# Kernel optimization log

Measured on AMD Instinct MI355X. Metric: run time of the kernel, lower is better.

The kernel has to match this reference:

```python
import jax, jax.numpy as jnp
import numpy as np

N_NODES = 50000
D = 128
L = 3  # layers
R = 4  # relations
E = 200000  # edges per relation
LN_EPS = 1e-5
NEG_SLOPE = 0.2


def setup_inputs() -> dict:
    key = jax.random.key(0)
    ks = jax.random.split(key, 12)
    s = 1.0 / np.sqrt(D)  # xavier-ish scale
    return {
        "h": jax.random.normal(ks[0], (N_NODES, D), jnp.float32),
        "edge_src": jax.random.randint(ks[1], (R, E), 0, N_NODES, jnp.int32),
        "edge_dst": jax.random.randint(ks[2], (R, E), 0, N_NODES, jnp.int32),
        "W_src": jax.random.normal(ks[3], (L, R, D, D), jnp.float32) * s,
        "W_dst": jax.random.normal(ks[4], (L, R, D, D), jnp.float32) * s,
        "attn_l": jax.random.normal(ks[5], (L, R, D), jnp.float32) * s,
        "attn_r": jax.random.normal(ks[6], (L, R, D), jnp.float32) * s,
        "gat_bias": jax.random.normal(ks[7], (L, R, D), jnp.float32) * 0.02,
        "ntype_bias": jax.random.normal(ks[8], (L, D), jnp.float32) * 0.02,
        "ln_gamma": jnp.ones((L, D), jnp.float32),
        "ln_beta": jnp.zeros((L, D), jnp.float32),
    }


def _gat_rel(x, Wsrc, Wdst, al, ar, b, src, dst):
    # single-head DGL GATConv with bipartite (src, dst) feats (same node set here)
    n = x.shape[0]
    hs = x @ Wsrc  # [N, D] projected source feats
    hd = x @ Wdst  # [N, D] projected dest feats
    el = (hs * al).sum(-1)  # [N]
    er = (hd * ar).sum(-1)  # [N]
    e = jax.nn.leaky_relu(el[src] + er[dst], NEG_SLOPE)  # [E]
    # edge softmax over incoming edges of each dst node
    m = jax.lax.stop_gradient(jax.ops.segment_max(e, dst, num_segments=n))
    a = jnp.exp(e - m[dst])
    denom = jax.ops.segment_sum(a, dst, num_segments=n)
    w = a / denom[dst]  # [E] attention weights
    out = jax.ops.segment_sum(hs[src] * w[:, None], dst, num_segments=n)  # [N, D]
    return out + b


def _layer_norm(x, g, b):
    mu = x.mean(-1, keepdims=True)
    var = ((x - mu) ** 2).mean(-1, keepdims=True)
    return (x - mu) * jax.lax.rsqrt(var + LN_EPS) * g + b


def reference(h, edge_src, edge_dst, W_src, W_dst, attn_l, attn_r,
              gat_bias, ntype_bias, ln_gamma, ln_beta):
    x = h
    n_layers = W_src.shape[0]
    gat_vmapped = jax.vmap(_gat_rel, in_axes=(None, 0, 0, 0, 0, 0, 0, 0))
    for l in range(n_layers):
        rel_out = gat_vmapped(x, W_src[l], W_dst[l], attn_l[l], attn_r[l],
                              gat_bias[l], edge_src, edge_dst)  # [R, N, D]
        hsum = rel_out.sum(0) + ntype_bias[l]  # HeteroGraphConv 'sum' + ntype bias
        if l < n_layers - 1:
            hsum = jax.nn.relu(hsum)  # activation on all but final layer
        # mean over heads (num_heads=1) is identity; then per-layer LayerNorm
        x = _layer_norm(hsum, ln_gamma[l], ln_beta[l])
    return x
```

## Files before the change

### kernel.cpp

```cpp
#include <hip/hip_runtime.h>

#define NN 50000
#define DIM 128
#define NREL 4
#define NEDGE 200000
#define NLAYER 3
#define SNB 196
#define GR 128
#define NTILE (NN / 16)

typedef short s16x8 __attribute__((ext_vector_type(8)));
typedef float f32x4 __attribute__((ext_vector_type(4)));

__device__ __forceinline__ unsigned short f2bf(float f) {
    union { float f; unsigned u; } c; c.f = f;
    unsigned u = c.u + 0x7fffu + ((c.u >> 16) & 1u);
    return (unsigned short)(u >> 16);
}
__device__ __forceinline__ float lo_bf(unsigned u) {
    union { float f; unsigned u; } c; c.u = u << 16; return c.f;
}
__device__ __forceinline__ float hi_bf(unsigned u) {
    union { float f; unsigned u; } c; c.u = u & 0xffff0000u; return c.f;
}

__global__ __launch_bounds__(256) void k_constf(float* __restrict__ out, int n, float v) {
    int i = blockIdx.x * 256 + threadIdx.x;
    if (i < n) out[i] = v;
}

__global__ __launch_bounds__(256) void k_count(const int* __restrict__ dst, int* __restrict__ counts) {
    int r = blockIdx.y;
    int i = blockIdx.x * 256 + threadIdx.x;
    if (i < NEDGE) {
        int d = dst[r * NEDGE + i];
        if ((unsigned)d < NN) atomicAdd(&counts[r * NN + d], 1);
    }
}

__global__ __launch_bounds__(256) void k_s1(const int* __restrict__ counts, int* __restrict__ bsum) {
    int r = blockIdx.y, b = blockIdx.x;
    int i = b * 256 + threadIdx.x;
    int v = (i < NN) ? counts[r * NN + i] : 0;
    #pragma unroll
    for (int m = 1; m < 64; m <<= 1) v += __shfl_xor(v, m);
    __shared__ int ws[4];
    int wid = threadIdx.x >> 6, lane = threadIdx.x & 63;
    if (lane == 0) ws[wid] = v;
    __syncthreads();
    if (threadIdx.x == 0) bsum[r * SNB + b] = ws[0] + ws[1] + ws[2] + ws[3];
}

__global__ __launch_bounds__(256) void k_s2(const int* __restrict__ bsum, int* __restrict__ boff) {
    int r = threadIdx.x >> 6;
    int lane = threadIdx.x & 63;
    int carry = 0;
    for (int c0 = 0; c0 < SNB; c0 += 64) {
        int b = c0 + lane;
        int v = (b < SNB) ? bsum[r * SNB + b] : 0;
        int inc = v;
        #pragma unroll
        for (int d = 1; d < 64; d <<= 1) {
            int t = __shfl_up(inc, d);
            if (lane >= d) inc += t;
        }
        if (b < SNB) boff[r * SNB + b] = carry + inc - v;
        carry += __shfl(inc, 63);
    }
}

__global__ __launch_bounds__(256) void k_s3(const int* __restrict__ counts, const int* __restrict__ boff,
                                            int* __restrict__ row_ptr, int* __restrict__ nxt) {
    int r = blockIdx.y, b = blockIdx.x;
    int i = b * 256 + threadIdx.x;
    int v = (i < NN) ? counts[r * NN + i] : 0;
    int lane = threadIdx.x & 63, wid = threadIdx.x >> 6;
    int inc = v;
    #pragma unroll
    for (int d = 1; d < 64; d <<= 1) {
        int t = __shfl_up(inc, d);
        if (lane >= d) inc += t;
    }
    __shared__ int ws[4];
    if (lane == 63) ws[wid] = inc;
    __syncthreads();
    int woff = 0;
    #pragma unroll
    for (int w = 0; w < 4; ++w) woff += (w < wid) ? ws[w] : 0;
    if (i < NN) {
        int ex = boff[r * SNB + b] + woff + inc - v;
        row_ptr[r * (NN + 1) + i] = ex;
        nxt[r * NN + i] = ex;
    }
    if (b == 0 && threadIdx.x == 0) row_ptr[r * (NN + 1) + NN] = NEDGE;
}

__global__ __launch_bounds__(256) void k_fill(const int* __restrict__ src, const int* __restrict__ dst,
                                              int* __restrict__ nxt, int* __restrict__ csr) {
    int r = blockIdx.y;
    int i = blockIdx.x * 256 + threadIdx.x;
    if (i < NEDGE) {
        int d = dst[r * NEDGE + i];
        if ((unsigned)d >= NN) return;
        int pos = atomicAdd(&nxt[r * NN + d], 1);
        if ((unsigned)pos < NEDGE) csr[r * NEDGE + pos] = src[r * NEDGE + i];
    }
}

__global__ __launch_bounds__(256) void k_prep(const float* __restrict__ Wsrc,
                                              const float* __restrict__ Wdst,
                                              const float* __restrict__ al,
                                              const float* __restrict__ ar,
                                              const float* __restrict__ ntb,
                                              const float* __restrict__ gb,
                                              const float* __restrict__ x,
                                              unsigned short* __restrict__ wf,
                                              float* __restrict__ wl,
                                              float* __restrict__ wr,
                                              float* __restrict__ biasc,
                                              unsigned short* __restrict__ xb) {
    int b = blockIdx.x;
    const int PL = NLAYER * 512;
    if (b < PL) {
        int l = b / 512;
        int t = b % 512;
        if (t < 256) {
            int idx = t * 256 + threadIdx.x;
            int jj = idx & 7, lane = (idx >> 3) & 63, s = (idx >> 9) & 3, tt = (idx >> 11) & 7, r = idx >> 14;
            int k = s * 32 + ((lane >> 4) << 3) + jj;
            int n = tt * 16 + (lane & 15);
            wf[l * 65536 + idx] = f2bf(Wsrc[((size_t)(l * NREL + r) * DIM + k) * DIM + n]);
        } else if (t < 384) {
            int gw = (t - 256) * 4 + (threadIdx.x >> 6);
            int lane = threadIdx.x & 63;
            int r = gw >> 7, k = gw & 127;
            const float* wrow = Wsrc + (((size_t)(l * NREL + r) * DIM + k) * DIM);
            const float* arow = al + (l * NREL + r) * DIM;
            float s = wrow[lane * 2] * arow[lane * 2] + wrow[lane * 2 + 1] * arow[lane * 2 + 1];
            #pragma unroll
            for (int m = 1; m < 64; m <<= 1) s += __shfl_xor(s, m);
            if (lane == 0) wl[l * 512 + gw] = s;
        } else {
            int gw = (t - 384) * 4 + (threadIdx.x >> 6);
            int lane = threadIdx.x & 63;
            int r = gw >> 7, k = gw & 127;
            const float* wrow = Wdst + (((size_t)(l * NREL + r) * DIM + k) * DIM);
            const float* arow = ar + (l * NREL + r) * DIM;
            float s = wrow[lane * 2] * arow[lane * 2] + wrow[lane * 2 + 1] * arow[lane * 2 + 1];
            #pragma unroll
            for (int m = 1; m < 64; m <<= 1) s += __shfl_xor(s, m);
            if (lane == 0) wr[l * 512 + gw] = s;
        }
    } else if (b < PL + 2) {
        int t = (b - PL) * 256 + threadIdx.x;
        if (t < NLAYER * DIM) {
            int l = t >> 7, k = t & 127;
            float s = ntb[t];
            #pragma unroll
            for (int r = 0; r < NREL; ++r) s += gb[(l * NREL + r) * DIM + k];
            biasc[t] = s;
        }
    } else {
        int i = ((b - PL - 2) * 256 + threadIdx.x) * 4;
        f32x4 v = *(const f32x4*)(x + i);
        unsigned short o[4];
        #pragma unroll
        for (int j = 0; j < 4; ++j) o[j] = f2bf(v[j]);
        *(ushort2*)(xb + i) = make_ushort2(o[0], o[1]);
        *(ushort2*)(xb + i + 2) = make_ushort2(o[2], o[3]);
    }
}

__global__ __launch_bounds__(256) void k_er0(const float* __restrict__ x,
                                             const float* __restrict__ wl,
                                             const float* __restrict__ wr,
                                             float* __restrict__ el,
                                             float* __restrict__ er) {
    int oct = threadIdx.x >> 3, ol = threadIdx.x & 7;
    int n = blockIdx.x * 32 + oct;
    if (n >= NN) return;
    int f0 = ol * 16;
    const float* xp = x + (size_t)n * DIM + f0;
    f32x4 xv[4];
    #pragma unroll
    for (int k = 0; k < 4; ++k) xv[k] = *(const f32x4*)(xp + 4 * k);
    #pragma unroll
    for (int r = 0; r < NREL; ++r) {
        float sl = 0.f, sr = 0.f;
        #pragma unroll
        for (int k = 0; k < 4; ++k) {
            f32x4 lv = *(const f32x4*)(wl + r * DIM + f0 + 4 * k);
            f32x4 rv = *(const f32x4*)(wr + r * DIM + f0 + 4 * k);
            sl += xv[k][0] * lv[0] + xv[k][1] * lv[1] + xv[k][2] * lv[2] + xv[k][3] * lv[3];
            sr += xv[k][0] * rv[0] + xv[k][1] * rv[1] + xv[k][2] * rv[2] + xv[k][3] * rv[3];
        }
        sl += __shfl_xor(sl, 1); sl += __shfl_xor(sl, 2); sl += __shfl_xor(sl, 4);
        sr += __shfl_xor(sr, 1); sr += __shfl_xor(sr, 2); sr += __shfl_xor(sr, 4);
        if (ol == 0) { el[r * NN + n] = sl; er[r * NN + n] = sr; }
    }
}

__global__ __launch_bounds__(256) void k_gather(const unsigned short* __restrict__ xb,
                                                const float* __restrict__ el,
                                                const float* __restrict__ er,
                                                const int* __restrict__ row_ptr,
                                                const int* __restrict__ csr,
                                                unsigned short* __restrict__ aggf) {
    int gid = blockIdx.x * 256 + threadIdx.x;
    int ol = gid & 3;
    int p  = gid >> 2;
    int n  = p >> 2;
    int r  = p & 3;
    if (n >= NN) return;
    int f0 = ol * 32;

    int start = row_ptr[r * (NN + 1) + n];
    int end   = row_ptr[r * (NN + 1) + n + 1];
    if (start < 0) start = 0;
    if (end > NEDGE) end = NEDGE;
    int deg = end - start;

    float ern = er[r * NN + n];
    const int* cp = csr + r * NEDGE;
    const float* elp = el + r * NN;

    f32x4 av[8] = {{0,0,0,0},{0,0,0,0},{0,0,0,0},{0,0,0,0},
                   {0,0,0,0},{0,0,0,0},{0,0,0,0},{0,0,0,0}};
    float denom = 0.f;
    if (deg > 0) {
        int s0 = cp[start]; if ((unsigned)s0 >= NN) s0 = 0;
        float e0 = elp[s0];
        const uint4* hp = (const uint4*)(xb + (size_t)s0 * DIM + f0);
        uint4 xa = hp[0], xbv = hp[1], xc = hp[2], xd = hp[3];
        for (int e = 0; e < deg; ++e) {
            int i1 = start + e + 1; i1 = (i1 < end) ? i1 : start;
            int s1 = cp[i1]; if ((unsigned)s1 >= NN) s1 = 0;
            float e1 = elp[s1];
            const uint4* hp1 = (const uint4*)(xb + (size_t)s1 * DIM + f0);
            uint4 ya = hp1[0], yb = hp1[1], yc = hp1[2], yd = hp1[3];

            float ev = e0 + ern;
            ev = ev >= 0.f ? ev : 0.2f * ev;
            ev = fminf(fmaxf(ev, -60.f), 60.f);
            float pw = __expf(ev);
            denom += pw;
            av[0][0] += pw * lo_bf(xa.x); av[0][1] += pw * hi_bf(xa.x);
            av[0][2] += pw * lo_bf(xa.y); av[0][3] += pw * hi_bf(xa.y);
            av[1][0] += pw * lo_bf(xa.z); av[1][1] += pw * hi_bf(xa.z);
            av[1][2] += pw * lo_bf(xa.w); av[1][3] += pw * hi_bf(xa.w);
            av[2][0] += pw * lo_bf(xbv.x); av[2][1] += pw * hi_bf(xbv.x);
            av[2][2] += pw * lo_bf(xbv.y); av[2][3] += pw * hi_bf(xbv.y);
            av[3][0] += pw * lo_bf(xbv.z); av[3][1] += pw * hi_bf(xbv.z);
            av[3][2] += pw * lo_bf(xbv.w); av[3][3] += pw * hi_bf(xbv.w);
            av[4][0] += pw * lo_bf(xc.x); av[4][1] += pw * hi_bf(xc.x);
            av[4][2] += pw * lo_bf(xc.y); av[4][3] += pw * hi_bf(xc.y);
            av[5][0] += pw * lo_bf(xc.z); av[5][1] += pw * hi_bf(xc.z);
            av[5][2] += pw * lo_bf(xc.w); av[5][3] += pw * hi_bf(xc.w);
            av[6][0] += pw * lo_bf(xd.x); av[6][1] += pw * hi_bf(xd.x);
            av[6][2] += pw * lo_bf(xd.y); av[6][3] += pw * hi_bf(xd.y);
            av[7][0] += pw * lo_bf(xd.z); av[7][1] += pw * hi_bf(xd.z);
            av[7][2] += pw * lo_bf(xd.w); av[7][3] += pw * hi_bf(xd.w);
            e0 = e1; xa = ya; xbv = yb; xc = yc; xd = yd;
        }
    }
    float inv = (deg > 0) ? (1.0f / denom) : 0.f;
    s16x8* ap = (s16x8*)aggf + ((size_t)(n >> 4) * 16 + (r * 4 + ol)) * 64 + (n & 15);
    #pragma unroll
    for (int q = 0; q < 4; ++q) {
        s16x8 o;
        #pragma unroll
        for (int j = 0; j < 4; ++j) {
            o[j]     = (short)f2bf(av[2 * q][j] * inv);
            o[j + 4] = (short)f2bf(av[2 * q + 1][j] * inv);
        }
        ap[q * 16] = o;
    }
}

__global__ __launch_bounds__(256) void k_gemm(const unsigned short* __restrict__ aggf,
                                              const unsigned short* __restrict__ wf,
                                              const float* __restrict__ biasc,
                                              const float* __restrict__ lng,
                                              const float* __restrict__ lnb,
                                              const float* __restrict__ wl,
                                              const float* __restrict__ wr,
                                              float* __restrict__ dout,
                                              unsigned short* __restrict__ xb2,
                                              float* __restrict__ el2,
                                              float* __restrict__ er2,
                                              int l, int last) {
    __shared__ float Cl[GR * DIM];
    int tid = threadIdx.x;
    int wv = tid >> 6, lane = tid & 63;
    int quad = lane >> 4, n16 = lane & 15;
    int tile0 = blockIdx.x * (GR / 16);

    f32x4 acc0[8], acc1[8];
    #pragma unroll
    for (int rt = 0; rt < 8; ++rt) {
        acc0[rt] = (f32x4){0.f, 0.f, 0.f, 0.f};
        acc1[rt] = (f32x4){0.f, 0.f, 0.f, 0.f};
    }
    {
        const s16x8* wfp = (const s16x8*)wf + (size_t)l * NREL * 2048;
        const s16x8* af = (const s16x8*)aggf;
        int t0c = wv * 2, t1c = wv * 2 + 1;
        for (int sp = 0; sp < 16; ++sp) {
            const s16x8* wb = wfp + (size_t)(sp >> 2) * 2048;
            int sl = sp & 3;
            s16x8 b0 = wb[(t0c * 4 + sl) * 64 + lane];
            s16x8 b1 = wb[(t1c * 4 + sl) * 64 + lane];
            #pragma unroll
            for (int rt = 0; rt < 8; ++rt) {
                int tile = tile0 + rt;
                if (tile >= NTILE) tile = 0;
                s16x8 a = af[((size_t)tile * 16 + sp) * 64 + lane];
                acc0[rt] = __builtin_amdgcn_mfma_f32_16x16x32_bf16(a, b0, acc0[rt], 0, 0, 0);
                acc1[rt] = __builtin_amdgcn_mfma_f32_16x16x32_bf16(a, b1, acc1[rt], 0, 0, 0);
            }
        }
    }
    {
        int t0c = wv * 2, t1c = wv * 2 + 1;
        #pragma unroll
        for (int rt = 0; rt < 8; ++rt) {
            #pragma unroll
            for (int reg = 0; reg < 4; ++reg) {
                int row = rt * 16 + quad * 4 + reg;
                Cl[row * DIM + t0c * 16 + n16] = acc0[rt][reg];
                Cl[row * DIM + t1c * 16 + n16] = acc1[rt][reg];
            }
        }
    }
    __syncthreads();

    for (int it = 0; it < GR / 8; ++it) {
        int nd2 = it * 8 + (tid >> 5);
        int sub = tid & 31;
        int f   = sub * 4;
        int n2  = blockIdx.x * GR + nd2;
        if (n2 >= NN) continue;

        float t[4];
        #pragma unroll
        for (int j = 0; j < 4; ++j) t[j] = Cl[nd2 * DIM + f + j] + biasc[l * DIM + f + j];
        if (!last) {
            #pragma unroll
            for (int j = 0; j < 4; ++j) t[j] = fmaxf(t[j], 0.f);
        }
        float s1 = 0.f;
        #pragma unroll
        for (int j = 0; j < 4; ++j) s1 += t[j];
        s1 += __shfl_xor(s1, 1); s1 += __shfl_xor(s1, 2);
        s1 += __shfl_xor(s1, 4); s1 += __shfl_xor(s1, 8);
        s1 += __shfl_xor(s1, 16);
        float mean = s1 * (1.0f / 128.0f);
        float s2 = 0.f;
        #pragma unroll
        for (int j = 0; j < 4; ++j) { t[j] -= mean; s2 += t[j] * t[j]; }
        s2 += __shfl_xor(s2, 1); s2 += __shfl_xor(s2, 2);
        s2 += __shfl_xor(s2, 4); s2 += __shfl_xor(s2, 8);
        s2 += __shfl_xor(s2, 16);
        float rs = rsqrtf(s2 * (1.0f / 128.0f) + 1e-5f);

        float y[4];
        #pragma unroll
        for (int j = 0; j < 4; ++j)
            y[j] = t[j] * rs * lng[l * DIM + f + j] + lnb[l * DIM + f + j];

        if (last) {
            float* op = dout + (size_t)n2 * DIM + f;
            f32x4 v0;
            v0[0] = y[0]; v0[1] = y[1]; v0[2] = y[2]; v0[3] = y[3];
            *(f32x4*)op = v0;
        } else {
            unsigned pk0 = (unsigned)f2bf(y[0]) | ((unsigned)f2bf(y[1]) << 16);
            unsigned pk1 = (unsigned)f2bf(y[2]) | ((unsigned)f2bf(y[3]) << 16);
            uint2 v; v.x = pk0; v.y = pk1;
            *(uint2*)(xb2 + (size_t)n2 * DIM + f) = v;

            const float* wlp = wl + (l + 1) * 512;
            const float* wrp = wr + (l + 1) * 512;
            #pragma unroll
            for (int rp = 0; rp < NREL; ++rp) {
                float sl_ = 0.f, sr_ = 0.f;
                #pragma unroll
                for (int j = 0; j < 4; ++j) {
                    sl_ += y[j] * wlp[rp * DIM + f + j];
                    sr_ += y[j] * wrp[rp * DIM + f + j];
                }
                sl_ += __shfl_xor(sl_, 1); sl_ += __shfl_xor(sl_, 2);
                sl_ += __shfl_xor(sl_, 4); sl_ += __shfl_xor(sl_, 8);
                sl_ += __shfl_xor(sl_, 16);
                sr_ += __shfl_xor(sr_, 1); sr_ += __shfl_xor(sr_, 2);
                sr_ += __shfl_xor(sr_, 4); sr_ += __shfl_xor(sr_, 8);
                sr_ += __shfl_xor(sr_, 16);
                if (sub == 0) {
                    el2[rp * NN + n2] = sl_;
                    er2[rp * NN + n2] = sr_;
                }
            }
        }
    }
}

extern "C" void kernel_launch(void* const* d_in, const int* in_sizes, int n_in,
                              void* d_out, int out_size, void* d_ws, size_t ws_size,
                              hipStream_t stream) {
    const float* h        = (const float*)d_in[0];
    const int*   edge_src = (const int*)d_in[1];
    const int*   edge_dst = (const int*)d_in[2];
    const float* W_src    = (const float*)d_in[3];
    const float* W_dst    = (const float*)d_in[4];
    const float* attn_l   = (const float*)d_in[5];
    const float* attn_r   = (const float*)d_in[6];
    const float* gat_bias = (const float*)d_in[7];
    const float* ntype_b  = (const float*)d_in[8];
    const float* ln_g     = (const float*)d_in[9];
    const float* ln_b     = (const float*)d_in[10];

    if (n_in < 11) return;
    if (in_sizes[0] != NN * DIM) return;
    if (in_sizes[1] != NREL * NEDGE || in_sizes[2] != NREL * NEDGE) return;
    if (in_sizes[3] != NLAYER * NREL * DIM * DIM || in_sizes[4] != NLAYER * NREL * DIM * DIM) return;
    if (in_sizes[5] != NLAYER * NREL * DIM || in_sizes[6] != NLAYER * NREL * DIM) return;
    if (in_sizes[7] != NLAYER * NREL * DIM || in_sizes[8] != NLAYER * DIM) return;
    if (out_size != NN * DIM) return;

    auto align256 = [](size_t x) { return (x + 255) & ~(size_t)255; };
    size_t szElEr = align256((size_t)NREL * NN * 4);
    size_t szXbf  = align256((size_t)NN * DIM * 2);
    size_t szWlr  = align256((size_t)NLAYER * 512 * 4);
    size_t szBc   = align256((size_t)NLAYER * DIM * 4);
    size_t szWf   = align256((size_t)NLAYER * NREL * DIM * DIM * 2);
    size_t szRp   = align256((size_t)NREL * (NN + 1) * 4);
    size_t szNxt  = align256((size_t)NREL * NN * 4);
    size_t szCsr  = align256((size_t)NREL * NEDGE * 4);
    size_t szScn  = align256((size_t)NREL * SNB * 4) * 2;
    size_t szAgg  = align256((size_t)NN * 512 * 2);
    size_t need = 4 * szElEr + 2 * szXbf + 2 * szWlr + szBc + szWf + szRp + szNxt + szCsr + szScn + szAgg;

    if (ws_size < need) {
        k_constf<<<(NN * DIM + 255) / 256, 256, 0, stream>>>((float*)d_out, NN * DIM, 100.0f);
        return;
    }

    char* base = (char*)d_ws;
    size_t off = 0;
    auto alloc = [&](size_t bytes) -> char* { char* p = base + off; off += align256(bytes); return p; };

    float* el   = (float*)alloc((size_t)NREL * NN * 4);
    float* er   = (float*)alloc((size_t)NREL * NN * 4);
    float* el2  = (float*)alloc((size_t)NREL * NN * 4);
    float* er2  = (float*)alloc((size_t)NREL * NN * 4);
    unsigned short* xbf  = (unsigned short*)alloc((size_t)NN * DIM * 2);
    unsigned short* xbf2 = (unsigned short*)alloc((size_t)NN * DIM * 2);
    float* wl    = (float*)alloc((size_t)NLAYER * 512 * 4);
    float* wr    = (float*)alloc((size_t)NLAYER * 512 * 4);
    float* biasc = (float*)alloc((size_t)NLAYER * DIM * 4);
    unsigned short* wfrag = (unsigned short*)alloc((size_t)NLAYER * NREL * DIM * DIM * 2);
    int* rowp = (int*)alloc((size_t)NREL * (NN + 1) * 4);
    int* nxt  = (int*)alloc((size_t)NREL * NN * 4);
    int* csr  = (int*)alloc((size_t)NREL * NEDGE * 4);
    int* bsum = (int*)alloc((size_t)NREL * SNB * 4);
    int* boff = (int*)alloc((size_t)NREL * SNB * 4);
    unsigned short* aggf = (unsigned short*)alloc((size_t)NN * 512 * 2);

    (void)hipMemsetAsync(nxt, 0, (size_t)NREL * NN * 4, stream);
    k_count<<<dim3((NEDGE + 255) / 256, NREL), 256, 0, stream>>>(edge_dst, nxt);
    k_s1<<<dim3(SNB, NREL), 256, 0, stream>>>(nxt, bsum);
    k_s2<<<1, 256, 0, stream>>>(bsum, boff);
    k_s3<<<dim3(SNB, NREL), 256, 0, stream>>>(nxt, boff, rowp, nxt);
    k_fill<<<dim3((NEDGE + 255) / 256, NREL), 256, 0, stream>>>(edge_src, edge_dst, nxt, csr);
    k_prep<<<NLAYER * 512 + 2 + NN * DIM / 1024, 256, 0, stream>>>(
        W_src, W_dst, attn_l, attn_r, ntype_b, gat_bias, h, wfrag, wl, wr, biasc, xbf);
    k_er0<<<(NN + 31) / 32, 256, 0, stream>>>(h, wl, wr, el, er);

    float* dout = (float*)d_out;
    const int GATHER_BLK = (NN * NREL * 4 + 255) / 256;
    const int GEMM_BLK   = (NN + GR - 1) / GR;

    k_gather<<<GATHER_BLK, 256, 0, stream>>>(xbf, el, er, rowp, csr, aggf);
    k_gemm<<<GEMM_BLK, 256, 0, stream>>>(aggf, wfrag, biasc, ln_g, ln_b, wl, wr,
                                         dout, xbf2, el2, er2, 0, 0);
    k_gather<<<GATHER_BLK, 256, 0, stream>>>(xbf2, el2, er2, rowp, csr, aggf);
    k_gemm<<<GEMM_BLK, 256, 0, stream>>>(aggf, wfrag, biasc, ln_g, ln_b, wl, wr,
                                         dout, xbf, el, er, 1, 0);
    k_gather<<<GATHER_BLK, 256, 0, stream>>>(xbf, el, er, rowp, csr, aggf);
    k_gemm<<<GEMM_BLK, 256, 0, stream>>>(aggf, wfrag, biasc, ln_g, ln_b, wl, wr,
                                         dout, xbf2, el2, er2, 2, 1);
}
```

Measured before the change: 434.2 us.

## Give each wave a full 16-row tile and fuse LayerNorm on accumulators

The GEMM kernel now assigns one 16-node tile per wave that covers all 128 output columns, instead of each block computing 128 rows with waves splitting columns. Bias, ReLU, LayerNorm and the attention dot products are done directly from MFMA accumulator registers using 16-lane shuffles, so the 64KB shared-memory staging buffer and the block barrier go away. This raises occupancy and removes the LDS round-trip. In exchange, every wave reloads the whole weight matrix from cache instead of sharing it across 8 row tiles, and the output stores become strided 2- and 4-byte writes rather than vectorised ones.

```diff
diff --git a/kernel.cpp b/kernel.cpp
--- a/kernel.cpp
+++ b/kernel.cpp
@@ -6,7 +6,6 @@
 #define NEDGE 200000
 #define NLAYER 3
 #define SNB 196
-#define GR 128
 #define NTILE (NN / 16)
 
 typedef short s16x8 __attribute__((ext_vector_type(8)));
@@ -289,113 +288,89 @@
                                               float* __restrict__ el2,
                                               float* __restrict__ er2,
                                               int l, int last) {
-    __shared__ float Cl[GR * DIM];
     int tid = threadIdx.x;
     int wv = tid >> 6, lane = tid & 63;
     int quad = lane >> 4, n16 = lane & 15;
-    int tile0 = blockIdx.x * (GR / 16);
-
-    f32x4 acc0[8], acc1[8];
-    #pragma unroll
-    for (int rt = 0; rt < 8; ++rt) {
-        acc0[rt] = (f32x4){0.f, 0.f, 0.f, 0.f};
-        acc1[rt] = (f32x4){0.f, 0.f, 0.f, 0.f};
-    }
-    {
-        const s16x8* wfp = (const s16x8*)wf + (size_t)l * NREL * 2048;
-        const s16x8* af = (const s16x8*)aggf;
-        int t0c = wv * 2, t1c = wv * 2 + 1;
-        for (int sp = 0; sp < 16; ++sp) {
-            const s16x8* wb = wfp + (size_t)(sp >> 2) * 2048;
-            int sl = sp & 3;
-            s16x8 b0 = wb[(t0c * 4 + sl) * 64 + lane];
-            s16x8 b1 = wb[(t1c * 4 + sl) * 64 + lane];
-            #pragma unroll
-            for (int rt = 0; rt < 8; ++rt) {
-                int tile = tile0 + rt;
-                if (tile >= NTILE) tile = 0;
-                s16x8 a = af[((size_t)tile * 16 + sp) * 64 + lane];
-                acc0[rt] = __builtin_amdgcn_mfma_f32_16x16x32_bf16(a, b0, acc0[rt], 0, 0, 0);
-                acc1[rt] = __builtin_amdgcn_mfma_f32_16x16x32_bf16(a, b1, acc1[rt], 0, 0, 0);
-            }
-        }
-    }
-    {
-        int t0c = wv * 2, t1c = wv * 2 + 1;
-        #pragma unroll
-        for (int rt = 0; rt < 8; ++rt) {
-            #pragma unroll
-            for (int reg = 0; reg < 4; ++reg) {
-                int row = rt * 16 + quad * 4 + reg;
-                Cl[row * DIM + t0c * 16 + n16] = acc0[rt][reg];
-                Cl[row * DIM + t1c * 16 + n16] = acc1[rt][reg];
-            }
-        }
-    }
-    __syncthreads();
-
-    for (int it = 0; it < GR / 8; ++it) {
-        int nd2 = it * 8 + (tid >> 5);
-        int sub = tid & 31;
-        int f   = sub * 4;
-        int n2  = blockIdx.x * GR + nd2;
-        if (n2 >= NN) continue;
-
-        float t[4];
-        #pragma unroll
-        for (int j = 0; j < 4; ++j) t[j] = Cl[nd2 * DIM + f + j] + biasc[l * DIM + f + j];
-        if (!last) {
-            #pragma unroll
-            for (int j = 0; j < 4; ++j) t[j] = fmaxf(t[j], 0.f);
-        }
+    int tile = blockIdx.x * 4 + wv;
+    int tclamp = (tile < NTILE) ? tile : 0;
+    int valid = (tile < NTILE);
+
+    const s16x8* wfp = (const s16x8*)wf + (size_t)l * NREL * 2048;
+    const s16x8* af  = (const s16x8*)aggf + (size_t)tclamp * 16 * 64;
+
+    f32x4 acc[8];
+    #pragma unroll
+    for (int t = 0; t < 8; ++t) acc[t] = (f32x4){0.f, 0.f, 0.f, 0.f};
+
+    for (int sp = 0; sp < 16; ++sp) {
+        s16x8 a = af[sp * 64 + lane];
+        const s16x8* wb = wfp + (size_t)(sp >> 2) * 2048;
+        int sl = sp & 3;
+        #pragma unroll
+        for (int t = 0; t < 8; ++t) {
+            s16x8 b = wb[(t * 4 + sl) * 64 + lane];
+            acc[t] = __builtin_amdgcn_mfma_f32_16x16x32_bf16(a, b, acc[t], 0, 0, 0);
+        }
+    }
+
+    float bv[8], gv[8], bbv[8];
+    #pragma unroll
+    for (int t = 0; t < 8; ++t) {
+        bv[t]  = biasc[l * DIM + t * 16 + n16];
+        gv[t]  = lng[l * DIM + t * 16 + n16];
+        bbv[t] = lnb[l * DIM + t * 16 + n16];
+    }
+    const float* wlp = wl + (l + 1) * 512;
+    const float* wrp = wr + (l + 1) * 512;
+
+    #pragma unroll
+    for (int reg = 0; reg < 4; ++reg) {
+        int n2 = tile * 16 + quad * 4 + reg;
+        float y[8];
         float s1 = 0.f;
         #pragma unroll
-        for (int j = 0; j < 4; ++j) s1 += t[j];
+        for (int t = 0; t < 8; ++t) {
+            float v = acc[t][reg] + bv[t];
+            if (!last) v = fmaxf(v, 0.f);
+            y[t] = v; s1 += v;
+        }
         s1 += __shfl_xor(s1, 1); s1 += __shfl_xor(s1, 2);
         s1 += __shfl_xor(s1, 4); s1 += __shfl_xor(s1, 8);
-        s1 += __shfl_xor(s1, 16);
         float mean = s1 * (1.0f / 128.0f);
         float s2 = 0.f;
         #pragma unroll
-        for (int j = 0; j < 4; ++j) { t[j] -= mean; s2 += t[j] * t[j]; }
+        for (int t = 0; t < 8; ++t) { y[t] -= mean; s2 += y[t] * y[t]; }
         s2 += __shfl_xor(s2, 1); s2 += __shfl_xor(s2, 2);
         s2 += __shfl_xor(s2, 4); s2 += __shfl_xor(s2, 8);
-        s2 += __shfl_xor(s2, 16);
         float rs = rsqrtf(s2 * (1.0f / 128.0f) + 1e-5f);
-
-        float y[4];
-        #pragma unroll
-        for (int j = 0; j < 4; ++j)
-            y[j] = t[j] * rs * lng[l * DIM + f + j] + lnb[l * DIM + f + j];
-
-        if (last) {
-            float* op = dout + (size_t)n2 * DIM + f;
-            f32x4 v0;
-            v0[0] = y[0]; v0[1] = y[1]; v0[2] = y[2]; v0[3] = y[3];
-            *(f32x4*)op = v0;
-        } else {
-            unsigned pk0 = (unsigned)f2bf(y[0]) | ((unsigned)f2bf(y[1]) << 16);
-            unsigned pk1 = (unsigned)f2bf(y[2]) | ((unsigned)f2bf(y[3]) << 16);
-            uint2 v; v.x = pk0; v.y = pk1;
-            *(uint2*)(xb2 + (size_t)n2 * DIM + f) = v;
-
-            const float* wlp = wl + (l + 1) * 512;
-            const float* wrp = wr + (l + 1) * 512;
+        #pragma unroll
+        for (int t = 0; t < 8; ++t) y[t] = y[t] * rs * gv[t] + bbv[t];
+
+        if (valid) {
+            if (last) {
+                float* op = dout + (size_t)n2 * DIM + n16;
+                #pragma unroll
+                for (int t = 0; t < 8; ++t) op[t * 16] = y[t];
+            } else {
+                unsigned short* xp = xb2 + (size_t)n2 * DIM + n16;
+                #pragma unroll
+                for (int t = 0; t < 8; ++t) xp[t * 16] = f2bf(y[t]);
+            }
+        }
+        if (!last) {
             #pragma unroll
             for (int rp = 0; rp < NREL; ++rp) {
                 float sl_ = 0.f, sr_ = 0.f;
                 #pragma unroll
-                for (int j = 0; j < 4; ++j) {
-                    sl_ += y[j] * wlp[rp * DIM + f + j];
-                    sr_ += y[j] * wrp[rp * DIM + f + j];
+                for (int t = 0; t < 8; ++t) {
+                    sl_ += y[t] * wlp[rp * DIM + t * 16 + n16];
+                    sr_ += y[t] * wrp[rp * DIM + t * 16 + n16];
                 }
                 sl_ += __shfl_xor(sl_, 1); sl_ += __shfl_xor(sl_, 2);
                 sl_ += __shfl_xor(sl_, 4); sl_ += __shfl_xor(sl_, 8);
-                sl_ += __shfl_xor(sl_, 16);
                 sr_ += __shfl_xor(sr_, 1); sr_ += __shfl_xor(sr_, 2);
                 sr_ += __shfl_xor(sr_, 4); sr_ += __shfl_xor(sr_, 8);
-                sr_ += __shfl_xor(sr_, 16);
-                if (sub == 0) {
+                if (valid && n16 == 0) {
                     el2[rp * NN + n2] = sl_;
                     er2[rp * NN + n2] = sr_;
                 }
@@ -478,7 +453,7 @@
 
     float* dout = (float*)d_out;
     const int GATHER_BLK = (NN * NREL * 4 + 255) / 256;
-    const int GEMM_BLK   = (NN + GR - 1) / GR;
+    const int GEMM_BLK   = (NTILE + 3) / 4;
 
     k_gather<<<GATHER_BLK, 256, 0, stream>>>(xbf, el, er, rowp, csr, aggf);
     k_gemm<<<GEMM_BLK, 256, 0, stream>>>(aggf, wfrag, biasc, ln_g, ln_b, wl, wr,
```

Result: faster. 404.4 us (-6.9%).
